# Kernel optimization log

Measured on AMD Instinct MI355X. Metric: run time of the kernel, lower is better.

Reference implementation:

```python
import jax, jax.numpy as jnp
import numpy as np
import math

D, H, NQP, NKP = 512, 8, 4, 4
DH = D // H
OUT_DIM = D + H * NKP * 3  # 608


def setup_inputs() -> dict:
    key = jax.random.key(0)
    ks = jax.random.split(key, 12)
    B, L = 2, 1024
    s = jax.random.normal(ks[0], (B, L, D), dtype=jnp.float32)
    R = jax.random.normal(ks[1], (B, L, 3, 3), dtype=jnp.float32)
    tr = jax.random.normal(ks[2], (B, L, 3), dtype=jnp.float32)
    sc = 0.02
    Wq = jax.random.normal(ks[3], (D, D), dtype=jnp.float32) * sc
    Wk = jax.random.normal(ks[4], (D, D), dtype=jnp.float32) * sc
    Wv = jax.random.normal(ks[5], (D, D), dtype=jnp.float32) * sc
    Wqp = jax.random.normal(ks[6], (D, H * NQP * 3), dtype=jnp.float32) * sc
    Wkp = jax.random.normal(ks[7], (D, H * NKP * 3), dtype=jnp.float32) * sc
    Wvp = jax.random.normal(ks[8], (D, H * NKP * 3), dtype=jnp.float32) * sc
    Wo = jax.random.normal(ks[9], (OUT_DIM, D), dtype=jnp.float32) * sc
    bo = jnp.zeros((D,), dtype=jnp.float32)
    gamma = jnp.ones((D,), dtype=jnp.float32)
    beta = jnp.zeros((D,), dtype=jnp.float32)
    w_C = jnp.full((H,), math.log(20.0), dtype=jnp.float32)
    return dict(s=s, R=R, tr=tr, Wq=Wq, Wk=Wk, Wv=Wv, Wqp=Wqp, Wkp=Wkp,
                Wvp=Wvp, Wo=Wo, bo=bo, gamma=gamma, beta=beta, w_C=w_C)


def _layernorm(x, gamma, beta, eps=1e-5):
    mu = jnp.mean(x, axis=-1, keepdims=True)
    var = jnp.var(x, axis=-1, keepdims=True)
    return (x - mu) * jax.lax.rsqrt(var + eps) * gamma + beta


def reference(s, R, tr, Wq, Wk, Wv, Wqp, Wkp, Wvp, Wo, bo, gamma, beta, w_C):
    B, L, _ = s.shape
    # scalar q/k/v: (B, L, H, dh)
    Q = (s @ Wq).reshape(B, L, H, DH)
    K = (s @ Wk).reshape(B, L, H, DH)
    V = (s @ Wv).reshape(B, L, H, DH)
    a_s = jnp.einsum('bihd,bjhd->bhij', Q, K) / math.sqrt(DH)
    # local points: (B, L, H, P, 3)
    Qp = (s @ Wqp).reshape(B, L, H, NQP, 3)
    Kp = (s @ Wkp).reshape(B, L, H, NKP, 3)
    Vp = (s @ Wvp).reshape(B, L, H, NKP, 3)
    tr_e = tr[:, :, None, None, :]
    to_global = lambda p: jnp.einsum('blxy,blhpy->blhpx', R, p) + tr_e
    Qp_g, Kp_g, Vp_g = to_global(Qp), to_global(Kp), to_global(Vp)
    # (B, H, L, P, 3)
    qh = jnp.transpose(Qp_g, (0, 2, 1, 3, 4))
    kh = jnp.transpose(Kp_g, (0, 2, 1, 3, 4))
    diff = qh[:, :, :, None] - kh[:, :, None]          # (B,H,L,L,P,3)
    sq_dist = jnp.sum(diff * diff, axis=(-2, -1))      # (B,H,L,L)
    wc = jax.nn.softplus(w_C)[None, :, None, None]
    attn = jax.nn.softmax(a_s - 0.5 * wc * sq_dist, axis=-1)
    out_s = jnp.einsum('bhij,bjhd->bihd', attn, V).reshape(B, L, D)
    Vp_agg = jnp.einsum('bhij,bjhpc->bihpc', attn, Vp_g)  # (B,L,H,P,3)
    # global -> local: R^T (p - tr)
    Vp_local = jnp.einsum('blyx,blhpy->blhpx', R, Vp_agg - tr_e)
    out_p = Vp_local.reshape(B, L, H * NKP * 3)
    out = jnp.concatenate([out_s, out_p], axis=-1) @ Wo + bo
    return _layernorm(s + out, gamma, beta)
```

## Files before the change

kernel.cpp:

```cpp
#include <hip/hip_runtime.h>
#include <hip/hip_fp16.h>
#include <math.h>

typedef _Float16 f16;
typedef _Float16 f16x8 __attribute__((ext_vector_type(8)));
typedef _Float16 f16x4v __attribute__((ext_vector_type(4)));
typedef float f32x4 __attribute__((ext_vector_type(4)));

#define BATCH   2
#define LSEQ    1024
#define BLTOT   2048
#define DMODEL  512
#define NHEAD   8
#define PDIM    1824
#define AW      96
#define VW      80
#define ODIM    608
#define NSPLIT  2
#define OCPSTR  1310720

__global__ __launch_bounds__(256)
void prep_kernel(const float* __restrict__ s,
                 const float* __restrict__ Wq, const float* __restrict__ Wk,
                 const float* __restrict__ Wv, const float* __restrict__ Wqp,
                 const float* __restrict__ Wkp, const float* __restrict__ Wvp,
                 const float* __restrict__ Wo,
                 f16* __restrict__ sH, f16* __restrict__ WallT, f16* __restrict__ WoT)
{
    const int blk = blockIdx.x;
    const int t = threadIdx.x;
    __shared__ float tile[32][33];

    if (blk < 1024) {
        const int i = blk * 256 + t;
        float4 v = ((const float4*)s)[i];
        f16x4v o = { (f16)v.x, (f16)v.y, (f16)v.z, (f16)v.w };
        ((f16x4v*)sH)[i] = o;
        return;
    }
    if (blk < 1936) {
        const int idx = blk - 1024;
        const int n0 = (idx % 57) * 32, k0 = (idx / 57) * 32;
        const float* src; int ld, nc0;
        if      (n0 < 512)  { src = Wq;  ld = 512; nc0 = n0; }
        else if (n0 < 1024) { src = Wk;  ld = 512; nc0 = n0 - 512; }
        else if (n0 < 1536) { src = Wv;  ld = 512; nc0 = n0 - 1024; }
        else if (n0 < 1632) { src = Wqp; ld = 96;  nc0 = n0 - 1536; }
        else if (n0 < 1728) { src = Wkp; ld = 96;  nc0 = n0 - 1632; }
        else                { src = Wvp; ld = 96;  nc0 = n0 - 1728; }
#pragma unroll
        for (int i = 0; i < 4; ++i) {
            const int idx2 = t + i * 256;
            const int kl = idx2 >> 5, nl = idx2 & 31;
            tile[kl][nl] = src[(long long)(k0 + kl) * ld + nc0 + nl];
        }
        __syncthreads();
#pragma unroll
        for (int i = 0; i < 4; ++i) {
            const int idx2 = t + i * 256;
            const int nl = idx2 >> 5, kl = idx2 & 31;
            WallT[(long long)(n0 + nl) * 512 + k0 + kl] = (f16)tile[kl][nl];
        }
        return;
    }
    {
        const int idx = blk - 1936;
        const int n0 = (idx % 16) * 32, k0 = (idx / 16) * 32;
#pragma unroll
        for (int i = 0; i < 4; ++i) {
            const int idx2 = t + i * 256;
            const int kl = idx2 >> 5, nl = idx2 & 31;
            tile[kl][nl] = Wo[(long long)(k0 + kl) * 512 + n0 + nl];
        }
        __syncthreads();
#pragma unroll
        for (int i = 0; i < 4; ++i) {
            const int idx2 = t + i * 256;
            const int nl = idx2 >> 5, kl = idx2 & 31;
            WoT[(long long)(n0 + nl) * 608 + k0 + kl] = (f16)tile[kl][nl];
        }
    }
}

template<int BN, bool OUT16>
__global__ __launch_bounds__(256)
void gemm2_kernel(const f16* __restrict__ A, const f16* __restrict__ Bt,
                  void* __restrict__ Cout, int K, int ldc)
{
    constexpr int BCH = (BN * 4 + 255) / 256;
    __shared__ f16 As[2][64][40];
    __shared__ f16 Bs[2][BN][40];
    const int t = threadIdx.x;
    const int w = t >> 6, lane = t & 63, l15 = lane & 15, lhi = lane >> 4;
    const int row0 = blockIdx.y * 64, col0 = blockIdx.x * BN;
    const int ar = t >> 2, ac = t & 3;

    f32x4 acc[BN / 16];
#pragma unroll
    for (int n = 0; n < BN / 16; ++n) acc[n] = (f32x4){0.f, 0.f, 0.f, 0.f};

    const int nsteps = K >> 5;

    f16x8 aR;
    f16x8 bR[BCH];
    aR = *(const f16x8*)&A[(long long)(row0 + ar) * K + ac * 8];
#pragma unroll
    for (int i = 0; i < BCH; ++i) {
        const int cid = t + i * 256;
        if (cid < BN * 4) {
            const int br = cid >> 2, bc = cid & 3;
            bR[i] = *(const f16x8*)&Bt[(long long)(col0 + br) * K + bc * 8];
        }
    }
    *(f16x8*)&As[0][ar][ac * 8] = aR;
#pragma unroll
    for (int i = 0; i < BCH; ++i) {
        const int cid = t + i * 256;
        if (cid < BN * 4) *(f16x8*)&Bs[0][cid >> 2][(cid & 3) * 8] = bR[i];
    }
    __syncthreads();

    for (int st = 0; st < nsteps; ++st) {
        const int cur = st & 1;
        if (st + 1 < nsteps) {
            const int k0 = (st + 1) << 5;
            aR = *(const f16x8*)&A[(long long)(row0 + ar) * K + k0 + ac * 8];
#pragma unroll
            for (int i = 0; i < BCH; ++i) {
                const int cid = t + i * 256;
                if (cid < BN * 4) {
                    const int br = cid >> 2, bc = cid & 3;
                    bR[i] = *(const f16x8*)&Bt[(long long)(col0 + br) * K + k0 + bc * 8];
                }
            }
        }
        f16x8 af = *(const f16x8*)&As[cur][w * 16 + l15][lhi * 8];
        f16x8 bf[BN / 16];
#pragma unroll
        for (int n = 0; n < BN / 16; ++n)
            bf[n] = *(const f16x8*)&Bs[cur][n * 16 + l15][lhi * 8];
#pragma unroll
        for (int n = 0; n < BN / 16; ++n)
            acc[n] = __builtin_amdgcn_mfma_f32_16x16x32_f16(af, bf[n], acc[n], 0, 0, 0);
        if (st + 1 < nsteps) {
            *(f16x8*)&As[cur ^ 1][ar][ac * 8] = aR;
#pragma unroll
            for (int i = 0; i < BCH; ++i) {
                const int cid = t + i * 256;
                if (cid < BN * 4) *(f16x8*)&Bs[cur ^ 1][cid >> 2][(cid & 3) * 8] = bR[i];
            }
        }
        __syncthreads();
    }

    const int row = row0 + w * 16 + lhi * 4;
#pragma unroll
    for (int n = 0; n < BN / 16; ++n) {
        const int col = col0 + n * 16 + l15;
#pragma unroll
        for (int r = 0; r < 4; ++r) {
            if (OUT16) ((f16*)Cout)[(long long)(row + r) * ldc + col] = (f16)acc[n][r];
            else       ((float*)Cout)[(long long)(row + r) * ldc + col] = acc[n][r];
        }
    }
}

__global__ __launch_bounds__(256)
void build_aug2_kernel(const f16* __restrict__ P, const float* __restrict__ Rm,
                       const float* __restrict__ tr, const float* __restrict__ wC,
                       f16* __restrict__ QA, f16* __restrict__ KA,
                       f16* __restrict__ VCT, float* __restrict__ KOFF)
{
    const int l0 = blockIdx.x * 64;
    const int bh = blockIdx.y;
    const int b = bh >> 3, h = bh & 7;
    const int t = threadIdx.x;

    __shared__ float Rl[64][9];
    __shared__ float trl[64][3];
    __shared__ f16 gq[64][12];
    __shared__ f16 gk[64][12];
    __shared__ float k2[64][4];
    __shared__ f16 Vt[VW][72];
    __shared__ float wcs;

    const long long blbase = (long long)b * LSEQ + l0;

    for (int i = t; i < 64 * 9; i += 256) Rl[i / 9][i % 9] = Rm[blbase * 9 + i];
    for (int i = t; i < 64 * 3; i += 256) trl[i / 3][i % 3] = tr[blbase * 3 + i];
    if (t == 0) { float x = wC[h]; wcs = log1pf(expf(x)); }
    __syncthreads();
    const float wc = wcs;

    for (int i = t; i < 768; i += 256) {
        const int l = i / 12, pp = i - l * 12;
        const int proj = pp >> 2, p = pp & 3;
        const f16* src = P + (blbase + l) * PDIM + 1536 + proj * 96 + h * 12 + p * 3;
        const float x = (float)src[0], y = (float)src[1], z = (float)src[2];
        const float gx = Rl[l][0]*x + Rl[l][1]*y + Rl[l][2]*z + trl[l][0];
        const float gy = Rl[l][3]*x + Rl[l][4]*y + Rl[l][5]*z + trl[l][1];
        const float gz = Rl[l][6]*x + Rl[l][7]*y + Rl[l][8]*z + trl[l][2];
        if (proj == 0) {
            gq[l][p * 3 + 0] = (f16)(wc * gx);
            gq[l][p * 3 + 1] = (f16)(wc * gy);
            gq[l][p * 3 + 2] = (f16)(wc * gz);
        } else if (proj == 1) {
            gk[l][p * 3 + 0] = (f16)gx;
            gk[l][p * 3 + 1] = (f16)gy;
            gk[l][p * 3 + 2] = (f16)gz;
            k2[l][p] = gx * gx + gy * gy + gz * gz;
        } else {
            Vt[64 + p * 3 + 0][l] = (f16)gx;
            Vt[64 + p * 3 + 1][l] = (f16)gy;
            Vt[64 + p * 3 + 2][l] = (f16)gz;
        }
    }
    for (int i = t; i < 512; i += 256) {
        const int l = i >> 3, ch = i & 7;
        f16x8 v = *(const f16x8*)&P[(blbase + l) * PDIM + 1024 + h * 64 + ch * 8];
#pragma unroll
        for (int j = 0; j < 8; ++j) Vt[ch * 8 + j][l] = v[j];
    }
    for (int i = t; i < 36; i += 256) {
        const int r = 76 + i / 9, ch = i % 9;
        *(f16x8*)&Vt[r][ch * 8] = (f16x8){0,0,0,0,0,0,0,0};
    }
    __syncthreads();

    if (t < 64)
        KOFF[(long long)bh * LSEQ + l0 + t] =
            0.5f * wc * (k2[t][0] + k2[t][1] + k2[t][2] + k2[t][3]);

    for (int i = t; i < 768; i += 256) {
        const int l = i / 12, ch = i - l * 12;
        const long long prow = (blbase + l) * PDIM;
        const long long orow = ((long long)bh * LSEQ + l0 + l) * AW;
        f16x8 q, k;
        if (ch < 8) {
            f16x8 qv = *(const f16x8*)&P[prow + h * 64 + ch * 8];
            f16x8 kv = *(const f16x8*)&P[prow + 512 + h * 64 + ch * 8];
            q = qv * (f16)0.125f;
            k = kv;
        } else if (ch == 8) {
#pragma unroll
            for (int j = 0; j < 8; ++j) { q[j] = gq[l][j]; k[j] = gk[l][j]; }
        } else if (ch == 9) {
#pragma unroll
            for (int j = 0; j < 8; ++j) {
                q[j] = (j < 4) ? gq[l][8 + j] : (f16)0.f;
                k[j] = (j < 4) ? gk[l][8 + j] : (f16)0.f;
            }
        } else {
            q = (f16x8){0,0,0,0,0,0,0,0};
            k = (f16x8){0,0,0,0,0,0,0,0};
        }
        *(f16x8*)&QA[orow + ch * 8] = q;
        *(f16x8*)&KA[orow + ch * 8] = k;
    }
    for (int i = t; i < 640; i += 256) {
        const int c = i >> 3, lg = i & 7;
        *(f16x8*)&VCT[((long long)bh * VW + c) * LSEQ + l0 + lg * 8] =
            *(const f16x8*)&Vt[c][lg * 8];
    }
}

__global__ __launch_bounds__(256, 2)
void attn_kernel(const f16* __restrict__ QA, const f16* __restrict__ KA,
                 const f16* __restrict__ VCT, const float* __restrict__ KOFF,
                 f16* __restrict__ OCp, float2* __restrict__ ML)
{
    const int bh = blockIdx.y;
    const int q0 = blockIdx.x * 64;
    const int z  = blockIdx.z;
    const int t = threadIdx.x;
    const int w = t >> 6, lane = t & 63, l15 = lane & 15, lhi = lane >> 4;

    __shared__ f16 Ks[128][104];
    __shared__ f16 Vs[VW][136];
    __shared__ f16 Ps[64][136];

    const f16* qbase = QA + ((long long)bh * LSEQ + q0 + w * 16 + l15) * AW;
    f16x8 qf[3];
#pragma unroll
    for (int ks = 0; ks < 3; ++ks)
        qf[ks] = *(const f16x8*)(qbase + ks * 32 + lhi * 8);

    f32x4 Oacc[5];
#pragma unroll
    for (int nv = 0; nv < 5; ++nv) Oacc[nv] = (f32x4){0.f, 0.f, 0.f, 0.f};
    float M[4], L[4];
#pragma unroll
    for (int r = 0; r < 4; ++r) { M[r] = -1e30f; L[r] = 0.f; }

    const f16* kgbase = KA + (long long)bh * LSEQ * AW;
    const f16* vgbase = VCT + (long long)bh * VW * LSEQ;
    const float* koffb = KOFF + (long long)bh * LSEQ;

    const int kvbeg = z * (LSEQ / NSPLIT);
    const int kvend = kvbeg + LSEQ / NSPLIT;

#pragma unroll
    for (int i = 0; i < 6; ++i) {
        const int cid = t + i * 256;
        const int r = cid / 12, c = cid - r * 12;
        *(f16x8*)&Ks[r][c * 8] = *(const f16x8*)(kgbase + (long long)(kvbeg + r) * AW + c * 8);
    }
#pragma unroll
    for (int i = 0; i < 5; ++i) {
        const int cid = t + i * 256;
        const int r = cid >> 4, c = cid & 15;
        *(f16x8*)&Vs[r][c * 8] = *(const f16x8*)(vgbase + (long long)r * LSEQ + kvbeg + c * 8);
    }
    __syncthreads();

    for (int kv0 = kvbeg; kv0 < kvend; kv0 += 128) {
        const bool more = (kv0 + 128 < kvend);
        f16x8 kpre[6], vpre[5];
        if (more) {
#pragma unroll
            for (int i = 0; i < 6; ++i) {
                const int cid = t + i * 256;
                const int r = cid / 12, c = cid - r * 12;
                kpre[i] = *(const f16x8*)(kgbase + (long long)(kv0 + 128 + r) * AW + c * 8);
            }
#pragma unroll
            for (int i = 0; i < 5; ++i) {
                const int cid = t + i * 256;
                const int r = cid >> 4, c = cid & 15;
                vpre[i] = *(const f16x8*)(vgbase + (long long)r * LSEQ + kv0 + 128 + c * 8);
            }
        }

        f32x4 sc[8];
#pragma unroll
        for (int n = 0; n < 8; ++n) sc[n] = (f32x4){0.f, 0.f, 0.f, 0.f};
        __builtin_amdgcn_s_setprio(1);
#pragma unroll
        for (int n = 0; n < 8; ++n)
#pragma unroll
            for (int ks = 0; ks < 3; ++ks) {
                f16x8 kb = *(const f16x8*)&Ks[n * 16 + l15][ks * 32 + lhi * 8];
                sc[n] = __builtin_amdgcn_mfma_f32_16x16x32_f16(qf[ks], kb, sc[n], 0, 0, 0);
            }
        __builtin_amdgcn_s_setprio(0);
#pragma unroll
        for (int n = 0; n < 8; ++n) {
            const float ko = koffb[kv0 + n * 16 + l15];
#pragma unroll
            for (int r = 0; r < 4; ++r) sc[n][r] -= ko;
        }
        float sscale[4];
#pragma unroll
        for (int r = 0; r < 4; ++r) {
            float mr = sc[0][r];
#pragma unroll
            for (int n = 1; n < 8; ++n) mr = fmaxf(mr, sc[n][r]);
#pragma unroll
            for (int off = 1; off < 16; off <<= 1) mr = fmaxf(mr, __shfl_xor(mr, off));
            const float nm = fmaxf(M[r], mr);
            sscale[r] = __expf(M[r] - nm);
            M[r] = nm;
        }
        float rsum[4] = {0.f, 0.f, 0.f, 0.f};
#pragma unroll
        for (int n = 0; n < 8; ++n)
#pragma unroll
            for (int r = 0; r < 4; ++r) {
                const float p = __expf(sc[n][r] - M[r]);
                sc[n][r] = p;
                rsum[r] += p;
            }
#pragma unroll
        for (int r = 0; r < 4; ++r) {
            float s = rsum[r];
#pragma unroll
            for (int off = 1; off < 16; off <<= 1) s += __shfl_xor(s, off);
            L[r] = L[r] * sscale[r] + s;
        }
#pragma unroll
        for (int nv = 0; nv < 5; ++nv)
#pragma unroll
            for (int r = 0; r < 4; ++r) Oacc[nv][r] *= sscale[r];

#pragma unroll
        for (int n = 0; n < 8; ++n)
#pragma unroll
            for (int r = 0; r < 4; ++r)
                Ps[w * 16 + lhi * 4 + r][n * 16 + l15] = (f16)sc[n][r];

        f16x8 pa[4];
#pragma unroll
        for (int ks = 0; ks < 4; ++ks)
            pa[ks] = *(const f16x8*)&Ps[w * 16 + l15][ks * 32 + lhi * 8];
        __builtin_amdgcn_s_setprio(1);
#pragma unroll
        for (int nv = 0; nv < 5; ++nv)
#pragma unroll
            for (int ks = 0; ks < 4; ++ks) {
                f16x8 vb = *(const f16x8*)&Vs[nv * 16 + l15][ks * 32 + lhi * 8];
                Oacc[nv] = __builtin_amdgcn_mfma_f32_16x16x32_f16(pa[ks], vb, Oacc[nv], 0, 0, 0);
            }
        __builtin_amdgcn_s_setprio(0);
        __syncthreads();

        if (more) {
#pragma unroll
            for (int i = 0; i < 6; ++i) {
                const int cid = t + i * 256;
                const int r = cid / 12, c = cid - r * 12;
                *(f16x8*)&Ks[r][c * 8] = kpre[i];
            }
#pragma unroll
            for (int i = 0; i < 5; ++i) {
                const int cid = t + i * 256;
                const int r = cid >> 4, c = cid & 15;
                *(f16x8*)&Vs[r][c * 8] = vpre[i];
            }
        }
        __syncthreads();
    }

    f16* obase = OCp + (((long long)(z * 16 + bh) * LSEQ) + q0 + w * 16 + lhi * 4) * VW;
#pragma unroll
    for (int nv = 0; nv < 5; ++nv)
#pragma unroll
        for (int r = 0; r < 4; ++r)
            obase[r * VW + nv * 16 + l15] = (f16)Oacc[nv][r];
    if (l15 == 0) {
#pragma unroll
        for (int r = 0; r < 4; ++r)
            ML[(long long)(z * 16 + bh) * LSEQ + q0 + w * 16 + lhi * 4 + r] =
                make_float2(M[r], L[r]);
    }
}

__global__ __launch_bounds__(256)
void combine_concat_kernel(const f16* __restrict__ OCp, const float2* __restrict__ ML,
                           const float* __restrict__ Rm, const float* __restrict__ tr,
                           f16* __restrict__ CC)
{
    const int bl0 = blockIdx.x * 4;
    const int b = bl0 >> 10;
    const int t = threadIdx.x;

    __shared__ float w1s[4][8], w2s[4][8];
    if (t < 32) {
        const int row = t >> 3, h = t & 7;
        const int l = (bl0 + row) & 1023;
        const int bh = b * 8 + h;
        const float2 m1 = ML[(long long)bh * LSEQ + l];
        const float2 m2 = ML[(long long)(16 + bh) * LSEQ + l];
        const float mm = fmaxf(m1.x, m2.x);
        const float e1 = __expf(m1.x - mm), e2 = __expf(m2.x - mm);
        const float inv = 1.0f / (m1.y * e1 + m2.y * e2);
        w1s[row][h] = e1 * inv; w2s[row][h] = e2 * inv;
    }
    __syncthreads();

    for (int idx = t; idx < 2048; idx += 256) {
        const int row = idx >> 9, c = idx & 511;
        const int h = c >> 6, ch = c & 63;
        const int l = (bl0 + row) & 1023;
        const long long base = ((long long)(b * 8 + h) * LSEQ + l) * VW + ch;
        const float v = w1s[row][h] * (float)OCp[base] + w2s[row][h] * (float)OCp[OCPSTR + base];
        CC[(long long)(bl0 + row) * ODIM + c] = (f16)v;
    }
    if (t < 128) {
        const int row = t >> 5, h = (t >> 2) & 7, p = t & 3;
        const int bl = bl0 + row, l = bl & 1023;
        const long long base = ((long long)(b * 8 + h) * LSEQ + l) * VW + 64 + p * 3;
        const float w1 = w1s[row][h], w2 = w2s[row][h];
        float o[3];
#pragma unroll
        for (int c = 0; c < 3; ++c)
            o[c] = w1 * (float)OCp[base + c] + w2 * (float)OCp[OCPSTR + base + c]
                 - tr[(long long)bl * 3 + c];
        const float* Rr = Rm + (long long)bl * 9;
        f16* crow = CC + (long long)bl * ODIM + 512 + h * 12 + p * 3;
        crow[0] = (f16)(Rr[0]*o[0] + Rr[3]*o[1] + Rr[6]*o[2]);
        crow[1] = (f16)(Rr[1]*o[0] + Rr[4]*o[1] + Rr[7]*o[2]);
        crow[2] = (f16)(Rr[2]*o[0] + Rr[5]*o[1] + Rr[8]*o[2]);
    }
}

__global__ __launch_bounds__(256)
void residual_ln_kernel(const float* __restrict__ s, const float* __restrict__ Y,
                        const float* __restrict__ bo, const float* __restrict__ gamma,
                        const float* __restrict__ beta, float* __restrict__ out)
{
    const int bl = blockIdx.x;
    const int t = threadIdx.x;
    const float* srow = s + (long long)bl * DMODEL;
    const float* yrow = Y + (long long)bl * DMODEL;

    const float v0 = srow[t]       + yrow[t]       + bo[t];
    const float v1 = srow[t + 256] + yrow[t + 256] + bo[t + 256];

    float sum = v0 + v1, sq = v0 * v0 + v1 * v1;
#pragma unroll
    for (int o = 32; o > 0; o >>= 1) {
        sum += __shfl_xor(sum, o);
        sq  += __shfl_xor(sq,  o);
    }
    __shared__ float rs[4], rq[4];
    const int wid = t >> 6, lane = t & 63;
    if (lane == 0) { rs[wid] = sum; rq[wid] = sq; }
    __syncthreads();
    sum = rs[0] + rs[1] + rs[2] + rs[3];
    sq  = rq[0] + rq[1] + rq[2] + rq[3];

    const float mu  = sum * (1.0f / DMODEL);
    const float var = sq * (1.0f / DMODEL) - mu * mu;
    const float inv = rsqrtf(var + 1e-5f);

    out[(long long)bl * DMODEL + t]       = (v0 - mu) * inv * gamma[t]       + beta[t];
    out[(long long)bl * DMODEL + t + 256] = (v1 - mu) * inv * gamma[t + 256] + beta[t + 256];
}

extern "C" void kernel_launch(void* const* d_in, const int* in_sizes, int n_in,
                              void* d_out, int out_size, void* d_ws, size_t ws_size,
                              hipStream_t stream)
{
    const float* s    = (const float*)d_in[0];
    const float* R    = (const float*)d_in[1];
    const float* tr   = (const float*)d_in[2];
    const float* Wq   = (const float*)d_in[3];
    const float* Wk   = (const float*)d_in[4];
    const float* Wv   = (const float*)d_in[5];
    const float* Wqp  = (const float*)d_in[6];
    const float* Wkp  = (const float*)d_in[7];
    const float* Wvp  = (const float*)d_in[8];
    const float* Wo   = (const float*)d_in[9];
    const float* bo   = (const float*)d_in[10];
    const float* gam  = (const float*)d_in[11];
    const float* bet  = (const float*)d_in[12];
    const float* wC   = (const float*)d_in[13];
    float* out = (float*)d_out;

    f16* sH    = (f16*)d_ws;
    f16* WallT = sH + 1048576;
    f16* WoT   = WallT + 933888;
    f16* P     = WoT + 311296;
    f16* QA    = P + 3735552;
    f16* KA    = QA + 1572864;
    f16* VCT   = KA + 1572864;
    float* KOFF = (float*)(VCT + 1310720);
    f16* OCp    = (f16*)(KOFF + 16384);
    float2* ML  = (float2*)(OCp + 2621440);
    f16* CC     = (f16*)(ML + 32768);
    float* Y    = (float*)(CC + 1245184);

    const dim3 blk(256);

    prep_kernel<<<dim3(2240), blk, 0, stream>>>(s, Wq, Wk, Wv, Wqp, Wkp, Wvp, Wo,
                                                sH, WallT, WoT);

    gemm2_kernel<96, true><<<dim3(19, 32), blk, 0, stream>>>(sH, WallT, P, 512, 1824);

    build_aug2_kernel<<<dim3(16, 16), blk, 0, stream>>>(P, R, tr, wC, QA, KA, VCT, KOFF);

    attn_kernel<<<dim3(16, 16, NSPLIT), blk, 0, stream>>>(QA, KA, VCT, KOFF, OCp, ML);

    combine_concat_kernel<<<dim3(512), blk, 0, stream>>>(OCp, ML, R, tr, CC);

    gemm2_kernel<64, false><<<dim3(8, 32), blk, 0, stream>>>(CC, WoT, Y, 608, 512);

    residual_ln_kernel<<<dim3(BLTOT), blk, 0, stream>>>(s, Y, bo, gam, bet, out);
}
```

Baseline: 72.69 us.

## Split attention KV into four chunks with 64-key tiles and higher occupancy

Doubles the flash-decoding style KV split from two to four, which doubles the attention grid, and halves the KV tile per iteration to 64 keys. LDS use drops and launch bounds ask for four blocks per SM, so more waves can hide latency across the 16x16x2 grid. The combine kernel now merges four partial results with a generalized max/sum rescale, and the workspace grows to hold them. The cost is extra partial output traffic, more combine work, and more loop iterations with syncs per block.

```diff
diff --git a/kernel.cpp b/kernel.cpp
--- a/kernel.cpp
+++ b/kernel.cpp
@@ -16,7 +16,8 @@
 #define AW      96
 #define VW      80
 #define ODIM    608
-#define NSPLIT  2
+#define NSPLIT  4
+#define KVBLK   64
 #define OCPSTR  1310720
 
 __global__ __launch_bounds__(256)
@@ -264,7 +265,7 @@
     }
 }
 
-__global__ __launch_bounds__(256, 2)
+__global__ __launch_bounds__(256, 4)
 void attn_kernel(const f16* __restrict__ QA, const f16* __restrict__ KA,
                  const f16* __restrict__ VCT, const float* __restrict__ KOFF,
                  f16* __restrict__ OCp, float2* __restrict__ ML)
@@ -275,9 +276,9 @@
     const int t = threadIdx.x;
     const int w = t >> 6, lane = t & 63, l15 = lane & 15, lhi = lane >> 4;
 
-    __shared__ f16 Ks[128][104];
-    __shared__ f16 Vs[VW][136];
-    __shared__ f16 Ps[64][136];
+    __shared__ f16 Ks[KVBLK][104];
+    __shared__ f16 Vs[VW][72];
+    __shared__ f16 Ps[64][72];
 
     const f16* qbase = QA + ((long long)bh * LSEQ + q0 + w * 16 + l15) * AW;
     f16x8 qf[3];
@@ -297,46 +298,50 @@
     const float* koffb = KOFF + (long long)bh * LSEQ;
 
     const int kvbeg = z * (LSEQ / NSPLIT);
-    const int kvend = kvbeg + LSEQ / NSPLIT;
-
-#pragma unroll
-    for (int i = 0; i < 6; ++i) {
+
+#pragma unroll
+    for (int i = 0; i < 3; ++i) {
         const int cid = t + i * 256;
         const int r = cid / 12, c = cid - r * 12;
         *(f16x8*)&Ks[r][c * 8] = *(const f16x8*)(kgbase + (long long)(kvbeg + r) * AW + c * 8);
     }
 #pragma unroll
-    for (int i = 0; i < 5; ++i) {
+    for (int i = 0; i < 3; ++i) {
         const int cid = t + i * 256;
-        const int r = cid >> 4, c = cid & 15;
-        *(f16x8*)&Vs[r][c * 8] = *(const f16x8*)(vgbase + (long long)r * LSEQ + kvbeg + c * 8);
+        if (cid < 640) {
+            const int r = cid >> 3, c = cid & 7;
+            *(f16x8*)&Vs[r][c * 8] = *(const f16x8*)(vgbase + (long long)r * LSEQ + kvbeg + c * 8);
+        }
     }
     __syncthreads();
 
-    for (int kv0 = kvbeg; kv0 < kvend; kv0 += 128) {
-        const bool more = (kv0 + 128 < kvend);
-        f16x8 kpre[6], vpre[5];
+    for (int it = 0; it < LSEQ / NSPLIT / KVBLK; ++it) {
+        const int kv0 = kvbeg + it * KVBLK;
+        const bool more = (it + 1 < LSEQ / NSPLIT / KVBLK);
+        f16x8 kpre[3], vpre[3];
         if (more) {
 #pragma unroll
-            for (int i = 0; i < 6; ++i) {
+            for (int i = 0; i < 3; ++i) {
                 const int cid = t + i * 256;
                 const int r = cid / 12, c = cid - r * 12;
-                kpre[i] = *(const f16x8*)(kgbase + (long long)(kv0 + 128 + r) * AW + c * 8);
-            }
-#pragma unroll
-            for (int i = 0; i < 5; ++i) {
+                kpre[i] = *(const f16x8*)(kgbase + (long long)(kv0 + KVBLK + r) * AW + c * 8);
+            }
+#pragma unroll
+            for (int i = 0; i < 3; ++i) {
                 const int cid = t + i * 256;
-                const int r = cid >> 4, c = cid & 15;
-                vpre[i] = *(const f16x8*)(vgbase + (long long)r * LSEQ + kv0 + 128 + c * 8);
-            }
-        }
-
-        f32x4 sc[8];
-#pragma unroll
-        for (int n = 0; n < 8; ++n) sc[n] = (f32x4){0.f, 0.f, 0.f, 0.f};
+                if (cid < 640) {
+                    const int r = cid >> 3, c = cid & 7;
+                    vpre[i] = *(const f16x8*)(vgbase + (long long)r * LSEQ + kv0 + KVBLK + c * 8);
+                }
+            }
+        }
+
+        f32x4 sc[4];
+#pragma unroll
+        for (int n = 0; n < 4; ++n) sc[n] = (f32x4){0.f, 0.f, 0.f, 0.f};
         __builtin_amdgcn_s_setprio(1);
 #pragma unroll
-        for (int n = 0; n < 8; ++n)
+        for (int n = 0; n < 4; ++n)
 #pragma unroll
             for (int ks = 0; ks < 3; ++ks) {
                 f16x8 kb = *(const f16x8*)&Ks[n * 16 + l15][ks * 32 + lhi * 8];
@@ -344,7 +349,7 @@
             }
         __builtin_amdgcn_s_setprio(0);
 #pragma unroll
-        for (int n = 0; n < 8; ++n) {
+        for (int n = 0; n < 4; ++n) {
             const float ko = koffb[kv0 + n * 16 + l15];
 #pragma unroll
             for (int r = 0; r < 4; ++r) sc[n][r] -= ko;
@@ -352,9 +357,7 @@
         float sscale[4];
 #pragma unroll
         for (int r = 0; r < 4; ++r) {
-            float mr = sc[0][r];
-#pragma unroll
-            for (int n = 1; n < 8; ++n) mr = fmaxf(mr, sc[n][r]);
+            float mr = fmaxf(fmaxf(sc[0][r], sc[1][r]), fmaxf(sc[2][r], sc[3][r]));
 #pragma unroll
             for (int off = 1; off < 16; off <<= 1) mr = fmaxf(mr, __shfl_xor(mr, off));
             const float nm = fmaxf(M[r], mr);
@@ -363,7 +366,7 @@
         }
         float rsum[4] = {0.f, 0.f, 0.f, 0.f};
 #pragma unroll
-        for (int n = 0; n < 8; ++n)
+        for (int n = 0; n < 4; ++n)
 #pragma unroll
             for (int r = 0; r < 4; ++r) {
                 const float p = __expf(sc[n][r] - M[r]);
@@ -383,20 +386,20 @@
             for (int r = 0; r < 4; ++r) Oacc[nv][r] *= sscale[r];
 
 #pragma unroll
-        for (int n = 0; n < 8; ++n)
+        for (int n = 0; n < 4; ++n)
 #pragma unroll
             for (int r = 0; r < 4; ++r)
                 Ps[w * 16 + lhi * 4 + r][n * 16 + l15] = (f16)sc[n][r];
 
-        f16x8 pa[4];
-#pragma unroll
-        for (int ks = 0; ks < 4; ++ks)
+        f16x8 pa[2];
+#pragma unroll
+        for (int ks = 0; ks < 2; ++ks)
             pa[ks] = *(const f16x8*)&Ps[w * 16 + l15][ks * 32 + lhi * 8];
         __builtin_amdgcn_s_setprio(1);
 #pragma unroll
         for (int nv = 0; nv < 5; ++nv)
 #pragma unroll
-            for (int ks = 0; ks < 4; ++ks) {
+            for (int ks = 0; ks < 2; ++ks) {
                 f16x8 vb = *(const f16x8*)&Vs[nv * 16 + l15][ks * 32 + lhi * 8];
                 Oacc[nv] = __builtin_amdgcn_mfma_f32_16x16x32_f16(pa[ks], vb, Oacc[nv], 0, 0, 0);
             }
@@ -405,22 +408,25 @@
 
         if (more) {
 #pragma unroll
-            for (int i = 0; i < 6; ++i) {
+            for (int i = 0; i < 3; ++i) {
                 const int cid = t + i * 256;
                 const int r = cid / 12, c = cid - r * 12;
                 *(f16x8*)&Ks[r][c * 8] = kpre[i];
             }
 #pragma unroll
-            for (int i = 0; i < 5; ++i) {
+            for (int i = 0; i < 3; ++i) {
                 const int cid = t + i * 256;
-                const int r = cid >> 4, c = cid & 15;
-                *(f16x8*)&Vs[r][c * 8] = vpre[i];
+                if (cid < 640) {
+                    const int r = cid >> 3, c = cid & 7;
+                    *(f16x8*)&Vs[r][c * 8] = vpre[i];
+                }
             }
         }
         __syncthreads();
     }
 
-    f16* obase = OCp + (((long long)(z * 16 + bh) * LSEQ) + q0 + w * 16 + lhi * 4) * VW;
+    f16* obase = OCp + (long long)z * OCPSTR
+               + (((long long)bh * LSEQ) + q0 + w * 16 + lhi * 4) * VW;
 #pragma unroll
     for (int nv = 0; nv < 5; ++nv)
 #pragma unroll
@@ -443,17 +449,29 @@
     const int b = bl0 >> 10;
     const int t = threadIdx.x;
 
-    __shared__ float w1s[4][8], w2s[4][8];
+    __shared__ float ws[4][8][NSPLIT];
     if (t < 32) {
         const int row = t >> 3, h = t & 7;
         const int l = (bl0 + row) & 1023;
         const int bh = b * 8 + h;
-        const float2 m1 = ML[(long long)bh * LSEQ + l];
-        const float2 m2 = ML[(long long)(16 + bh) * LSEQ + l];
-        const float mm = fmaxf(m1.x, m2.x);
-        const float e1 = __expf(m1.x - mm), e2 = __expf(m2.x - mm);
-        const float inv = 1.0f / (m1.y * e1 + m2.y * e2);
-        w1s[row][h] = e1 * inv; w2s[row][h] = e2 * inv;
+        float m[NSPLIT], lv[NSPLIT];
+        float mm = -1e30f;
+#pragma unroll
+        for (int sidx = 0; sidx < NSPLIT; ++sidx) {
+            const float2 v = ML[(long long)(sidx * 16 + bh) * LSEQ + l];
+            m[sidx] = v.x; lv[sidx] = v.y;
+            mm = fmaxf(mm, v.x);
+        }
+        float denom = 0.f;
+#pragma unroll
+        for (int sidx = 0; sidx < NSPLIT; ++sidx) {
+            const float e = __expf(m[sidx] - mm);
+            m[sidx] = e;
+            denom += lv[sidx] * e;
+        }
+        const float inv = 1.0f / denom;
+#pragma unroll
+        for (int sidx = 0; sidx < NSPLIT; ++sidx) ws[row][h][sidx] = m[sidx] * inv;
     }
     __syncthreads();
 
@@ -462,19 +480,25 @@
         const int h = c >> 6, ch = c & 63;
         const int l = (bl0 + row) & 1023;
         const long long base = ((long long)(b * 8 + h) * LSEQ + l) * VW + ch;
-        const float v = w1s[row][h] * (float)OCp[base] + w2s[row][h] * (float)OCp[OCPSTR + base];
+        float v = 0.f;
+#pragma unroll
+        for (int sidx = 0; sidx < NSPLIT; ++sidx)
+            v += ws[row][h][sidx] * (float)OCp[(long long)sidx * OCPSTR + base];
         CC[(long long)(bl0 + row) * ODIM + c] = (f16)v;
     }
     if (t < 128) {
         const int row = t >> 5, h = (t >> 2) & 7, p = t & 3;
         const int bl = bl0 + row, l = bl & 1023;
         const long long base = ((long long)(b * 8 + h) * LSEQ + l) * VW + 64 + p * 3;
-        const float w1 = w1s[row][h], w2 = w2s[row][h];
         float o[3];
 #pragma unroll
-        for (int c = 0; c < 3; ++c)
-            o[c] = w1 * (float)OCp[base + c] + w2 * (float)OCp[OCPSTR + base + c]
-                 - tr[(long long)bl * 3 + c];
+        for (int c = 0; c < 3; ++c) {
+            float v = 0.f;
+#pragma unroll
+            for (int sidx = 0; sidx < NSPLIT; ++sidx)
+                v += ws[row][h][sidx] * (float)OCp[(long long)sidx * OCPSTR + base + c];
+            o[c] = v - tr[(long long)bl * 3 + c];
+        }
         const float* Rr = Rm + (long long)bl * 9;
         f16* crow = CC + (long long)bl * ODIM + 512 + h * 12 + p * 3;
         crow[0] = (f16)(Rr[0]*o[0] + Rr[3]*o[1] + Rr[6]*o[2]);
@@ -546,8 +570,8 @@
     f16* VCT   = KA + 1572864;
     float* KOFF = (float*)(VCT + 1310720);
     f16* OCp    = (f16*)(KOFF + 16384);
-    float2* ML  = (float2*)(OCp + 2621440);
-    f16* CC     = (f16*)(ML + 32768);
+    float2* ML  = (float2*)(OCp + 4 * OCPSTR);
+    f16* CC     = (f16*)(ML + 65536);
     float* Y    = (float*)(CC + 1245184);
 
     const dim3 blk(256);
```

After: 76.01 us. 4.6% more time.

## Add lazy softmax rescaling, LSE-based split combine, and fold Wo transpose into projection

Applied to the files above, without the earlier changes.

The attention loop now skips the running-max update and the rescaling of the output accumulator when every row's new block max stays within a threshold of the current max. This removes exps and multiplies on most iterations at the cost of a wave-wide vote and branch. The attention kernel now normalizes its output and stores a log-sum-exp, which simplifies the split combine. The Wo transpose moves out of the prep kernel into extra blocks of a dedicated projection GEMM kernel, so it runs concurrently with the matmul and the prep launch shrinks.

```diff
diff --git a/kernel.cpp b/kernel.cpp
--- a/kernel.cpp
+++ b/kernel.cpp
@@ -24,8 +24,7 @@
                  const float* __restrict__ Wq, const float* __restrict__ Wk,
                  const float* __restrict__ Wv, const float* __restrict__ Wqp,
                  const float* __restrict__ Wkp, const float* __restrict__ Wvp,
-                 const float* __restrict__ Wo,
-                 f16* __restrict__ sH, f16* __restrict__ WallT, f16* __restrict__ WoT)
+                 f16* __restrict__ sH, f16* __restrict__ WallT)
 {
     const int blk = blockIdx.x;
     const int t = threadIdx.x;
@@ -38,7 +37,7 @@
         ((f16x4v*)sH)[i] = o;
         return;
     }
-    if (blk < 1936) {
+    {
         const int idx = blk - 1024;
         const int n0 = (idx % 57) * 32, k0 = (idx / 57) * 32;
         const float* src; int ld, nc0;
@@ -61,24 +60,110 @@
             const int nl = idx2 >> 5, kl = idx2 & 31;
             WallT[(long long)(n0 + nl) * 512 + k0 + kl] = (f16)tile[kl][nl];
         }
+    }
+}
+
+__global__ __launch_bounds__(256)
+void proj_kernel(const f16* __restrict__ A, const f16* __restrict__ Bt,
+                 const float* __restrict__ Wo, f16* __restrict__ WoT,
+                 f16* __restrict__ P)
+{
+    __shared__ f16 As[2][64][40];
+    __shared__ f16 Bs[2][96][40];
+    const int t = threadIdx.x;
+
+    if (blockIdx.y >= 32) {
+        float (*tile)[33] = (float(*)[33])&As[0][0][0];
+        const int base = (blockIdx.x + (blockIdx.y - 32) * 19) * 8;
+#pragma unroll 1
+        for (int it = 0; it < 8; ++it) {
+            const int idx = base + it;
+            const int n0 = (idx & 15) * 32, k0 = (idx >> 4) * 32;
+#pragma unroll
+            for (int i = 0; i < 4; ++i) {
+                const int idx2 = t + i * 256;
+                const int kl = idx2 >> 5, nl = idx2 & 31;
+                tile[kl][nl] = Wo[(long long)(k0 + kl) * 512 + n0 + nl];
+            }
+            __syncthreads();
+#pragma unroll
+            for (int i = 0; i < 4; ++i) {
+                const int idx2 = t + i * 256;
+                const int nl = idx2 >> 5, kl = idx2 & 31;
+                WoT[(long long)(n0 + nl) * 608 + k0 + kl] = (f16)tile[kl][nl];
+            }
+            __syncthreads();
+        }
         return;
     }
-    {
-        const int idx = blk - 1936;
-        const int n0 = (idx % 16) * 32, k0 = (idx / 16) * 32;
-#pragma unroll
-        for (int i = 0; i < 4; ++i) {
-            const int idx2 = t + i * 256;
-            const int kl = idx2 >> 5, nl = idx2 & 31;
-            tile[kl][nl] = Wo[(long long)(k0 + kl) * 512 + n0 + nl];
+
+    const int w = t >> 6, lane = t & 63, l15 = lane & 15, lhi = lane >> 4;
+    const int row0 = blockIdx.y * 64, col0 = blockIdx.x * 96;
+    const int ar = t >> 2, ac = t & 3;
+    const int K = 512;
+
+    f32x4 acc[6];
+#pragma unroll
+    for (int n = 0; n < 6; ++n) acc[n] = (f32x4){0.f, 0.f, 0.f, 0.f};
+
+    f16x8 aR, bR[2];
+    aR = *(const f16x8*)&A[(long long)(row0 + ar) * K + ac * 8];
+#pragma unroll
+    for (int i = 0; i < 2; ++i) {
+        const int cid = t + i * 256;
+        if (cid < 384) {
+            const int br = cid >> 2, bc = cid & 3;
+            bR[i] = *(const f16x8*)&Bt[(long long)(col0 + br) * K + bc * 8];
+        }
+    }
+    *(f16x8*)&As[0][ar][ac * 8] = aR;
+#pragma unroll
+    for (int i = 0; i < 2; ++i) {
+        const int cid = t + i * 256;
+        if (cid < 384) *(f16x8*)&Bs[0][cid >> 2][(cid & 3) * 8] = bR[i];
+    }
+    __syncthreads();
+
+    for (int st = 0; st < 16; ++st) {
+        const int cur = st & 1;
+        if (st + 1 < 16) {
+            const int k0 = (st + 1) << 5;
+            aR = *(const f16x8*)&A[(long long)(row0 + ar) * K + k0 + ac * 8];
+#pragma unroll
+            for (int i = 0; i < 2; ++i) {
+                const int cid = t + i * 256;
+                if (cid < 384) {
+                    const int br = cid >> 2, bc = cid & 3;
+                    bR[i] = *(const f16x8*)&Bt[(long long)(col0 + br) * K + k0 + bc * 8];
+                }
+            }
+        }
+        f16x8 af = *(const f16x8*)&As[cur][w * 16 + l15][lhi * 8];
+        f16x8 bf[6];
+#pragma unroll
+        for (int n = 0; n < 6; ++n)
+            bf[n] = *(const f16x8*)&Bs[cur][n * 16 + l15][lhi * 8];
+#pragma unroll
+        for (int n = 0; n < 6; ++n)
+            acc[n] = __builtin_amdgcn_mfma_f32_16x16x32_f16(af, bf[n], acc[n], 0, 0, 0);
+        if (st + 1 < 16) {
+            *(f16x8*)&As[cur ^ 1][ar][ac * 8] = aR;
+#pragma unroll
+            for (int i = 0; i < 2; ++i) {
+                const int cid = t + i * 256;
+                if (cid < 384) *(f16x8*)&Bs[cur ^ 1][cid >> 2][(cid & 3) * 8] = bR[i];
+            }
         }
         __syncthreads();
-#pragma unroll
-        for (int i = 0; i < 4; ++i) {
-            const int idx2 = t + i * 256;
-            const int nl = idx2 >> 5, kl = idx2 & 31;
-            WoT[(long long)(n0 + nl) * 608 + k0 + kl] = (f16)tile[kl][nl];
-        }
+    }
+
+    const int row = row0 + w * 16 + lhi * 4;
+#pragma unroll
+    for (int n = 0; n < 6; ++n) {
+        const int col = col0 + n * 16 + l15;
+#pragma unroll
+        for (int r = 0; r < 4; ++r)
+            P[(long long)(row + r) * PDIM + col] = (f16)acc[n][r];
     }
 }
 
@@ -267,7 +352,7 @@
 __global__ __launch_bounds__(256, 2)
 void attn_kernel(const f16* __restrict__ QA, const f16* __restrict__ KA,
                  const f16* __restrict__ VCT, const float* __restrict__ KOFF,
-                 f16* __restrict__ OCp, float2* __restrict__ ML)
+                 f16* __restrict__ OCp, float* __restrict__ LSE)
 {
     const int bh = blockIdx.y;
     const int q0 = blockIdx.x * 64;
@@ -349,38 +434,63 @@
 #pragma unroll
             for (int r = 0; r < 4; ++r) sc[n][r] -= ko;
         }
-        float sscale[4];
+        float mr[4];
 #pragma unroll
         for (int r = 0; r < 4; ++r) {
-            float mr = sc[0][r];
-#pragma unroll
-            for (int n = 1; n < 8; ++n) mr = fmaxf(mr, sc[n][r]);
-#pragma unroll
-            for (int off = 1; off < 16; off <<= 1) mr = fmaxf(mr, __shfl_xor(mr, off));
-            const float nm = fmaxf(M[r], mr);
-            sscale[r] = __expf(M[r] - nm);
-            M[r] = nm;
-        }
+            float m = sc[0][r];
+#pragma unroll
+            for (int n = 1; n < 8; ++n) m = fmaxf(m, sc[n][r]);
+#pragma unroll
+            for (int off = 1; off < 16; off <<= 1) m = fmaxf(m, __shfl_xor(m, off));
+            mr[r] = m;
+        }
+        const bool nog = (mr[0] <= M[0] + 8.f) && (mr[1] <= M[1] + 8.f) &&
+                         (mr[2] <= M[2] + 8.f) && (mr[3] <= M[3] + 8.f);
         float rsum[4] = {0.f, 0.f, 0.f, 0.f};
-#pragma unroll
-        for (int n = 0; n < 8; ++n)
+        if (__all(nog)) {
+#pragma unroll
+            for (int n = 0; n < 8; ++n)
+#pragma unroll
+                for (int r = 0; r < 4; ++r) {
+                    const float p = __expf(sc[n][r] - M[r]);
+                    sc[n][r] = p;
+                    rsum[r] += p;
+                }
 #pragma unroll
             for (int r = 0; r < 4; ++r) {
-                const float p = __expf(sc[n][r] - M[r]);
-                sc[n][r] = p;
-                rsum[r] += p;
-            }
-#pragma unroll
-        for (int r = 0; r < 4; ++r) {
-            float s = rsum[r];
-#pragma unroll
-            for (int off = 1; off < 16; off <<= 1) s += __shfl_xor(s, off);
-            L[r] = L[r] * sscale[r] + s;
-        }
-#pragma unroll
-        for (int nv = 0; nv < 5; ++nv)
-#pragma unroll
-            for (int r = 0; r < 4; ++r) Oacc[nv][r] *= sscale[r];
+                float s2 = rsum[r];
+#pragma unroll
+                for (int off = 1; off < 16; off <<= 1) s2 += __shfl_xor(s2, off);
+                L[r] += s2;
+            }
+        } else {
+            float sscale[4];
+#pragma unroll
+            for (int r = 0; r < 4; ++r) {
+                const float nm = fmaxf(M[r], mr[r]);
+                sscale[r] = __expf(M[r] - nm);
+                M[r] = nm;
+            }
+#pragma unroll
+            for (int n = 0; n < 8; ++n)
+#pragma unroll
+                for (int r = 0; r < 4; ++r) {
+                    const float p = __expf(sc[n][r] - M[r]);
+                    sc[n][r] = p;
+                    rsum[r] += p;
+                }
+#pragma unroll
+            for (int r = 0; r < 4; ++r) {
+                float s2 = rsum[r];
+#pragma unroll
+                for (int off = 1; off < 16; off <<= 1) s2 += __shfl_xor(s2, off);
+                L[r] = L[r] * sscale[r] + s2;
+            }
+#pragma unroll
+            for (int nv = 0; nv < 5; ++nv)
+#pragma unroll
+                for (int r = 0; r < 4; ++r) Oacc[nv][r] *= sscale[r];
+        }
 
 #pragma unroll
         for (int n = 0; n < 8; ++n)
@@ -420,22 +530,25 @@
         __syncthreads();
     }
 
+    float inv[4];
+#pragma unroll
+    for (int r = 0; r < 4; ++r) inv[r] = 1.0f / L[r];
     f16* obase = OCp + (((long long)(z * 16 + bh) * LSEQ) + q0 + w * 16 + lhi * 4) * VW;
 #pragma unroll
     for (int nv = 0; nv < 5; ++nv)
 #pragma unroll
         for (int r = 0; r < 4; ++r)
-            obase[r * VW + nv * 16 + l15] = (f16)Oacc[nv][r];
+            obase[r * VW + nv * 16 + l15] = (f16)(Oacc[nv][r] * inv[r]);
     if (l15 == 0) {
 #pragma unroll
         for (int r = 0; r < 4; ++r)
-            ML[(long long)(z * 16 + bh) * LSEQ + q0 + w * 16 + lhi * 4 + r] =
-                make_float2(M[r], L[r]);
+            LSE[(long long)(z * 16 + bh) * LSEQ + q0 + w * 16 + lhi * 4 + r] =
+                M[r] + __logf(L[r]);
     }
 }
 
 __global__ __launch_bounds__(256)
-void combine_concat_kernel(const f16* __restrict__ OCp, const float2* __restrict__ ML,
+void combine_concat_kernel(const f16* __restrict__ OCp, const float* __restrict__ LSE,
                            const float* __restrict__ Rm, const float* __restrict__ tr,
                            f16* __restrict__ CC)
 {
@@ -448,11 +561,11 @@
         const int row = t >> 3, h = t & 7;
         const int l = (bl0 + row) & 1023;
         const int bh = b * 8 + h;
-        const float2 m1 = ML[(long long)bh * LSEQ + l];
-        const float2 m2 = ML[(long long)(16 + bh) * LSEQ + l];
-        const float mm = fmaxf(m1.x, m2.x);
-        const float e1 = __expf(m1.x - mm), e2 = __expf(m2.x - mm);
-        const float inv = 1.0f / (m1.y * e1 + m2.y * e2);
+        const float l1 = LSE[(long long)bh * LSEQ + l];
+        const float l2 = LSE[(long long)(16 + bh) * LSEQ + l];
+        const float mm = fmaxf(l1, l2);
+        const float e1 = __expf(l1 - mm), e2 = __expf(l2 - mm);
+        const float inv = 1.0f / (e1 + e2);
         w1s[row][h] = e1 * inv; w2s[row][h] = e2 * inv;
     }
     __syncthreads();
@@ -546,22 +659,22 @@
     f16* VCT   = KA + 1572864;
     float* KOFF = (float*)(VCT + 1310720);
     f16* OCp    = (f16*)(KOFF + 16384);
-    float2* ML  = (float2*)(OCp + 2621440);
-    f16* CC     = (f16*)(ML + 32768);
+    float* LSE  = (float*)(OCp + 2621440);
+    f16* CC     = (f16*)(LSE + 32768);
     float* Y    = (float*)(CC + 1245184);
 
     const dim3 blk(256);
 
-    prep_kernel<<<dim3(2240), blk, 0, stream>>>(s, Wq, Wk, Wv, Wqp, Wkp, Wvp, Wo,
-                                                sH, WallT, WoT);
-
-    gemm2_kernel<96, true><<<dim3(19, 32), blk, 0, stream>>>(sH, WallT, P, 512, 1824);
+    prep_kernel<<<dim3(1936), blk, 0, stream>>>(s, Wq, Wk, Wv, Wqp, Wkp, Wvp,
+                                                sH, WallT);
+
+    proj_kernel<<<dim3(19, 34), blk, 0, stream>>>(sH, WallT, Wo, WoT, P);
 
     build_aug2_kernel<<<dim3(16, 16), blk, 0, stream>>>(P, R, tr, wC, QA, KA, VCT, KOFF);
 
-    attn_kernel<<<dim3(16, 16, NSPLIT), blk, 0, stream>>>(QA, KA, VCT, KOFF, OCp, ML);
-
-    combine_concat_kernel<<<dim3(512), blk, 0, stream>>>(OCp, ML, R, tr, CC);
+    attn_kernel<<<dim3(16, 16, NSPLIT), blk, 0, stream>>>(QA, KA, VCT, KOFF, OCp, LSE);
+
+    combine_concat_kernel<<<dim3(512), blk, 0, stream>>>(OCp, LSE, R, tr, CC);
 
     gemm2_kernel<64, false><<<dim3(8, 32), blk, 0, stream>>>(CC, WoT, Y, 608, 512);
 
```

After: 73.60 us. About the same (+1.2%).
